# Kernel tuning notes

Measured on AMD Instinct MI355X. Metric: run time of the kernel, lower is better.

Reference implementation:

```python
import jax, jax.numpy as jnp
import numpy as np

# Scalar-only irreps: 8x0e nodes in, 4x0e edge in, 8x0e edge out, 16x0e node out.
N = 50000          # nodes
E = 800000         # edges
MUL_NODE_IN = 8
MUL_EDGE_IN = 4
MUL_Z = 2 * MUL_NODE_IN          # cat([x[i], x[j]]) -> 16
MUL_EDGE_OUT = 8
MUL_NODE_OUT = 16
W_NUMEL = MUL_EDGE_IN * MUL_Z * MUL_EDGE_OUT  # 512 = edge_tp.weight_numel
RAD_IN, RAD_HID = 16, 64         # radial_neurons=[16, 64]


def setup_inputs() -> dict:
    key = jax.random.key(0)
    ks = jax.random.split(key, 7)
    x = jax.random.normal(ks[0], (N, MUL_NODE_IN), dtype=jnp.float32)
    edge_index = jax.random.randint(ks[1], (2, E), 0, N)
    edge_attr = jax.random.normal(ks[2], (E, MUL_EDGE_IN), dtype=jnp.float32)
    edge_len_emb = jax.random.normal(ks[3], (E, RAD_IN), dtype=jnp.float32)
    # radial MLP (e3nn FullyConnectedNet: normalized linear layers, silu)
    w1 = jax.random.normal(ks[4], (RAD_IN, RAD_HID), dtype=jnp.float32)
    w2 = jax.random.normal(ks[5], (RAD_HID, W_NUMEL), dtype=jnp.float32)
    # node_tp internal shared weights: [mul_node_in, mul_edge_out, mul_node_out]
    w_node = jax.random.normal(ks[6], (MUL_NODE_IN, MUL_EDGE_OUT, MUL_NODE_OUT), dtype=jnp.float32)
    return {"x": x, "edge_index": edge_index, "edge_attr": edge_attr,
            "edge_len_emb": edge_len_emb, "w1": w1, "w2": w2, "w_node": w_node}


def reference(x, edge_index, edge_attr, edge_len_emb, w1, w2, w_node):
    i, j = edge_index[0], edge_index[1]
    # radial MLP -> per-edge TP weights (e3nn normalized linears, silu)
    h = jax.nn.silu(edge_len_emb @ w1 / jnp.sqrt(jnp.float32(RAD_IN)))
    w_edge = (h @ w2 / jnp.sqrt(jnp.float32(RAD_HID)))
    w_edge = w_edge.reshape(E, MUL_EDGE_IN, MUL_Z, MUL_EDGE_OUT)
    # gather + concat: z = cat([x[i], x[j]])  [E, 16]
    z = jnp.concatenate([x[i], x[j]], axis=-1)
    # edge_tp: fully-connected scalar TP with path norm 1/sqrt(mul1*mul2)
    edge_out = jnp.einsum('ea,eb,eabk->ek', edge_attr, z, w_edge)
    edge_out = edge_out / jnp.sqrt(jnp.float32(MUL_EDGE_IN * MUL_Z))
    # scatter-sum to destination nodes j
    e_sum = jax.ops.segment_sum(edge_out, j, num_segments=x.shape[0])
    # node_tp: shared internal weights, path norm 1/sqrt(mul1*mul2)
    x_out = jnp.einsum('na,nb,abk->nk', x, e_sum, w_node)
    x_out = x_out / jnp.sqrt(jnp.float32(MUL_NODE_IN * MUL_EDGE_OUT))
    return (x_out, edge_out)
```

## Files before the change

kernel.cpp:

```cpp
#include <hip/hip_runtime.h>


typedef __attribute__((ext_vector_type(8))) short short8;
typedef __attribute__((ext_vector_type(4))) float floatx4;

__device__ inline unsigned short f2bf(float f) {
    union { float f; unsigned u; } v; v.f = f;
    unsigned r = v.u + 0x7FFFu + ((v.u >> 16) & 1u);
    return (unsigned short)(r >> 16);
}

__device__ inline unsigned cvt_pk_bf16(float lo, float hi) {
    unsigned r;
    asm("v_cvt_pk_bf16_f32 %0, %1, %2" : "=v"(r) : "v"(lo), "v"(hi));
    return r;
}

constexpr int TB   = 512;
constexpr int NBLK = 256;

constexpr int W2_LD  = 72;
constexpr int HS_LD  = 72;
constexpr int ZT_LDF = 48;
constexpr int AT_LDF = 32;

__global__ __launch_bounds__(TB, 2) void edge_kernel(
    const float* __restrict__ x,
    const int*   __restrict__ ei,
    const float* __restrict__ attr,
    const float* __restrict__ emb,
    const float* __restrict__ w1,
    const float* __restrict__ w2,
    float* __restrict__ edge_out,
    float* __restrict__ e_sum,
    int E)
{
    __shared__ __align__(16) unsigned short s_w2t[512 * W2_LD];
    __shared__ __align__(16) unsigned short s_hsA[8 * 32 * HS_LD];
    __shared__ __align__(16) float          s_ztA[8 * 16 * ZT_LDF];
    __shared__ __align__(16) float          s_atA[8 * 4 * AT_LDF];
    __shared__ int                          s_vjA[8 * 32];

    const int tid  = threadIdx.x;
    const int wave = tid >> 6;
    const int lane = tid & 63;
    const int m16  = lane & 15;
    const int quad = lane >> 4;
    const int par  = m16 >> 3;

    for (int idx = tid; idx < 512 * 64; idx += TB) {
        const int n = idx & 511, k = idx >> 9;
        s_w2t[n * W2_LD + k] = f2bf(w2[k * 512 + n]);
    }
    __syncthreads();

    short8 w1f[4];
    #pragma unroll
    for (int ct = 0; ct < 4; ++ct) {
        short8 f;
        if (quad < 2) {
            #pragma unroll
            for (int j = 0; j < 8; ++j)
                f[j] = (short)f2bf(w1[(quad * 8 + j) * 64 + ct * 16 + m16]);
        } else {
            #pragma unroll
            for (int j = 0; j < 8; ++j) f[j] = 0;
        }
        w1f[ct] = f;
    }

    unsigned short* hsw = s_hsA + wave * 32 * HS_LD;
    float*          ztw = s_ztA + wave * 16 * ZT_LDF;
    float*          atw = s_atA + wave * 4 * AT_LDF;
    int*            vjw = s_vjA + wave * 32;

    const int  wid = blockIdx.x * 8 + wave;
    const int  nw  = NBLK * 8;
    const int  ntiles = E >> 5;
    const bool stg = (quad < 2);
    const int  mst = quad * 16 + m16;

    float4 xi0, xi1, xj0, xj1, a4;
    float4 em0a, em0b, em1a, em1b;
    int viN = 0, vjN = 0, vjC = 0;

    if (wid < ntiles && stg) {
        const int e0 = (wid << 5) + mst;
        const int vi = ei[e0];
        vjC = ei[E + e0];
        xi0 = *(const float4*)(x + (size_t)vi * 8);
        xi1 = *(const float4*)(x + (size_t)vi * 8 + 4);
        xj0 = *(const float4*)(x + (size_t)vjC * 8);
        xj1 = *(const float4*)(x + (size_t)vjC * 8 + 4);
        a4  = *(const float4*)(attr + (size_t)e0 * 4);
        const float* ep0 = emb + (size_t)((wid << 5) + m16) * 16 + quad * 8;
        em0a = *(const float4*)ep0;
        em0b = *(const float4*)(ep0 + 4);
        const float* ep1 = emb + (size_t)((wid << 5) + 16 + m16) * 16 + quad * 8;
        em1a = *(const float4*)ep1;
        em1b = *(const float4*)(ep1 + 4);
        const int t1 = (wid + nw < ntiles) ? (wid + nw) : wid;
        const int e1 = (t1 << 5) + mst;
        viN = ei[e1];
        vjN = ei[E + e1];
    }

    for (int tile = wid; tile < ntiles; tile += nw) {
        const int base = tile << 5;

        if (stg) {
            ztw[ 0*ZT_LDF+mst]=xi0.x; ztw[ 1*ZT_LDF+mst]=xi0.y;
            ztw[ 2*ZT_LDF+mst]=xi0.z; ztw[ 3*ZT_LDF+mst]=xi0.w;
            ztw[ 4*ZT_LDF+mst]=xi1.x; ztw[ 5*ZT_LDF+mst]=xi1.y;
            ztw[ 6*ZT_LDF+mst]=xi1.z; ztw[ 7*ZT_LDF+mst]=xi1.w;
            ztw[ 8*ZT_LDF+mst]=xj0.x; ztw[ 9*ZT_LDF+mst]=xj0.y;
            ztw[10*ZT_LDF+mst]=xj0.z; ztw[11*ZT_LDF+mst]=xj0.w;
            ztw[12*ZT_LDF+mst]=xj1.x; ztw[13*ZT_LDF+mst]=xj1.y;
            ztw[14*ZT_LDF+mst]=xj1.z; ztw[15*ZT_LDF+mst]=xj1.w;
            atw[0*AT_LDF+mst]=a4.x;   atw[1*AT_LDF+mst]=a4.y;
            atw[2*AT_LDF+mst]=a4.z;   atw[3*AT_LDF+mst]=a4.w;
            vjw[mst] = vjC;
        }

        short8 a1[2];
        {
            union { short8 s8; unsigned u[4]; } uu;
            if (stg) {
                uu.u[0] = cvt_pk_bf16(em0a.x, em0a.y);
                uu.u[1] = cvt_pk_bf16(em0a.z, em0a.w);
                uu.u[2] = cvt_pk_bf16(em0b.x, em0b.y);
                uu.u[3] = cvt_pk_bf16(em0b.z, em0b.w);
            } else {
                uu.u[0]=0u; uu.u[1]=0u; uu.u[2]=0u; uu.u[3]=0u;
            }
            a1[0] = uu.s8;
            if (stg) {
                uu.u[0] = cvt_pk_bf16(em1a.x, em1a.y);
                uu.u[1] = cvt_pk_bf16(em1a.z, em1a.w);
                uu.u[2] = cvt_pk_bf16(em1b.x, em1b.y);
                uu.u[3] = cvt_pk_bf16(em1b.z, em1b.w);
            } else {
                uu.u[0]=0u; uu.u[1]=0u; uu.u[2]=0u; uu.u[3]=0u;
            }
            a1[1] = uu.s8;
        }

        {
            const int tn     = tile + nw;
            const int tn_cl  = (tn  < ntiles) ? tn  : tile;
            const int tnn    = tn + nw;
            const int tnn_cl = (tnn < ntiles) ? tnn : tn_cl;
            if (stg) {
                const int en = (tn_cl << 5) + mst;
                vjC = vjN;
                xi0 = *(const float4*)(x + (size_t)viN * 8);
                xi1 = *(const float4*)(x + (size_t)viN * 8 + 4);
                xj0 = *(const float4*)(x + (size_t)vjN * 8);
                xj1 = *(const float4*)(x + (size_t)vjN * 8 + 4);
                a4  = *(const float4*)(attr + (size_t)en * 4);
                const float* ep0 = emb + (size_t)((tn_cl << 5) + m16) * 16 + quad * 8;
                em0a = *(const float4*)ep0;
                em0b = *(const float4*)(ep0 + 4);
                const float* ep1 = emb + (size_t)((tn_cl << 5) + 16 + m16) * 16 + quad * 8;
                em1a = *(const float4*)ep1;
                em1b = *(const float4*)(ep1 + 4);
                const int enn = (tnn_cl << 5) + mst;
                viN = ei[enn];
                vjN = ei[E + enn];
            }
        }

        #pragma unroll
        for (int s = 0; s < 2; ++s) {
            #pragma unroll
            for (int ct = 0; ct < 4; ++ct) {
                floatx4 c = {0.f, 0.f, 0.f, 0.f};
                c = __builtin_amdgcn_mfma_f32_16x16x32_bf16(a1[s], w1f[ct], c, 0, 0, 0);
                float sv[4];
                #pragma unroll
                for (int r = 0; r < 4; ++r) {
                    const float u   = c[r] * 0.25f;
                    const float den = 1.f + __expf(-u);
                    sv[r] = u * __builtin_amdgcn_rcpf(den) * 0.015625f;
                }
                const unsigned p01 = cvt_pk_bf16(sv[0], sv[1]);
                const unsigned p23 = cvt_pk_bf16(sv[2], sv[3]);
                const int col  = ct * 16 + m16;
                const int row0 = s * 16 + quad * 4;
                hsw[(row0 + 0) * HS_LD + col] = (unsigned short)p01;
                hsw[(row0 + 1) * HS_LD + col] = (unsigned short)(p01 >> 16);
                hsw[(row0 + 2) * HS_LD + col] = (unsigned short)p23;
                hsw[(row0 + 3) * HS_LD + col] = (unsigned short)(p23 >> 16);
            }
        }

        short8 a2[2][2];
        #pragma unroll
        for (int s = 0; s < 2; ++s)
            #pragma unroll
            for (int q = 0; q < 2; ++q)
                a2[s][q] = *(const short8*)(hsw + (s * 16 + m16) * HS_LD + q * 32 + quad * 8);

        float eacc[2][4];
        #pragma unroll
        for (int s = 0; s < 2; ++s)
            #pragma unroll
            for (int r = 0; r < 4; ++r) eacc[s][r] = 0.f;

        __builtin_amdgcn_s_setprio(1);
        #pragma unroll 1
        for (int g = 0; g < 4; ++g) {
            float av[2][4];
            #pragma unroll
            for (int s = 0; s < 2; ++s) {
                const float4 a4v = *(const float4*)(atw + g * AT_LDF + s * 16 + quad * 4);
                av[s][0] = a4v.x; av[s][1] = a4v.y;
                av[s][2] = a4v.z; av[s][3] = a4v.w;
            }
            float tacc[2][4];
            #pragma unroll
            for (int s = 0; s < 2; ++s)
                #pragma unroll
                for (int r = 0; r < 4; ++r) tacc[s][r] = 0.f;

            #pragma unroll
            for (int tt = 0; tt < 8; ++tt) {
                const int t = g * 8 + tt;
                short8 b2[2];
                b2[0] = *(const short8*)(s_w2t + (16 * t + m16) * W2_LD + quad * 8);
                b2[1] = *(const short8*)(s_w2t + (16 * t + m16) * W2_LD + 32 + quad * 8);
                const int b_idx = (2 * tt + par) & 15;
                #pragma unroll
                for (int s = 0; s < 2; ++s) {
                    floatx4 c = {0.f, 0.f, 0.f, 0.f};
                    c = __builtin_amdgcn_mfma_f32_16x16x32_bf16(a2[s][0], b2[0], c, 0, 0, 0);
                    c = __builtin_amdgcn_mfma_f32_16x16x32_bf16(a2[s][1], b2[1], c, 0, 0, 0);
                    const float4 zv = *(const float4*)(ztw + b_idx * ZT_LDF + s * 16 + quad * 4);
                    tacc[s][0] = fmaf(c[0], zv.x, tacc[s][0]);
                    tacc[s][1] = fmaf(c[1], zv.y, tacc[s][1]);
                    tacc[s][2] = fmaf(c[2], zv.z, tacc[s][2]);
                    tacc[s][3] = fmaf(c[3], zv.w, tacc[s][3]);
                }
            }
            #pragma unroll
            for (int s = 0; s < 2; ++s)
                #pragma unroll
                for (int r = 0; r < 4; ++r)
                    eacc[s][r] = fmaf(av[s][r], tacc[s][r], eacc[s][r]);
        }
        __builtin_amdgcn_s_setprio(0);

        #pragma unroll
        for (int s = 0; s < 2; ++s)
            #pragma unroll
            for (int r = 0; r < 4; ++r)
                eacc[s][r] += __shfl_xor(eacc[s][r], 8, 64);

        if (m16 < 8) {
            #pragma unroll
            for (int s = 0; s < 2; ++s) {
                const int4 vjq = *(const int4*)(vjw + s * 16 + quad * 4);
                const int vjr[4] = {vjq.x, vjq.y, vjq.z, vjq.w};
                #pragma unroll
                for (int r = 0; r < 4; ++r) {
                    const int e = base + s * 16 + quad * 4 + r;
                    edge_out[(size_t)e * 8 + m16] = eacc[s][r];
                    atomicAdd(e_sum + (size_t)vjr[r] * 8 + m16, eacc[s][r]);
                }
            }
        }
    }
}

__global__ __launch_bounds__(256) void node_kernel(
    const float* __restrict__ x,
    const float* __restrict__ e_sum,
    const float* __restrict__ w_node,
    float* __restrict__ x_out,
    int N)
{
    __shared__ float s_w[8 * 8 * 16];
    for (int idx = threadIdx.x; idx < 1024; idx += 256) s_w[idx] = w_node[idx];
    __syncthreads();

    const int n = blockIdx.x * 256 + threadIdx.x;
    if (n >= N) return;

    float xa[8], eb[8];
    #pragma unroll
    for (int a = 0; a < 8; ++a) xa[a] = x[(size_t)n * 8 + a];
    #pragma unroll
    for (int b = 0; b < 8; ++b) eb[b] = e_sum[(size_t)n * 8 + b];

    float out[16];
    #pragma unroll
    for (int k = 0; k < 16; ++k) out[k] = 0.f;

    const float4* wv = (const float4*)s_w;
    #pragma unroll
    for (int a = 0; a < 8; ++a) {
        #pragma unroll
        for (int b = 0; b < 8; ++b) {
            const float t = xa[a] * eb[b] * 0.125f;
            #pragma unroll
            for (int k4 = 0; k4 < 4; ++k4) {
                const float4 w = wv[(a * 8 + b) * 4 + k4];
                out[k4 * 4 + 0] = fmaf(t, w.x, out[k4 * 4 + 0]);
                out[k4 * 4 + 1] = fmaf(t, w.y, out[k4 * 4 + 1]);
                out[k4 * 4 + 2] = fmaf(t, w.z, out[k4 * 4 + 2]);
                out[k4 * 4 + 3] = fmaf(t, w.w, out[k4 * 4 + 3]);
            }
        }
    }

    float4* xo = (float4*)(x_out + (size_t)n * 16);
    #pragma unroll
    for (int k4 = 0; k4 < 4; ++k4)
        xo[k4] = make_float4(out[k4 * 4 + 0], out[k4 * 4 + 1],
                             out[k4 * 4 + 2], out[k4 * 4 + 3]);
}

extern "C" void kernel_launch(void* const* d_in, const int* in_sizes, int n_in,
                              void* d_out, int out_size, void* d_ws, size_t ws_size,
                              hipStream_t stream) {
    const float* x      = (const float*)d_in[0];
    const int*   ei     = (const int*)d_in[1];
    const float* attr   = (const float*)d_in[2];
    const float* emb    = (const float*)d_in[3];
    const float* w1     = (const float*)d_in[4];
    const float* w2     = (const float*)d_in[5];
    const float* w_node = (const float*)d_in[6];

    const int N = in_sizes[0] / 8;
    const int E = in_sizes[2] / 4;

    float* x_out    = (float*)d_out;
    float* edge_out = (float*)d_out + (size_t)N * 16;
    float* e_sum    = (float*)d_ws;

    hipMemsetAsync(e_sum, 0, (size_t)N * 8 * sizeof(float), stream);

    edge_kernel<<<NBLK, TB, 0, stream>>>(x, ei, attr, emb, w1, w2,
                                         edge_out, e_sum, E);

    node_kernel<<<(N + 255) / 256, 256, 0, stream>>>(x, e_sum, w_node, x_out, N);
}
```

Before: 190.8 us.

## Cut edge kernel LDS via swizzled w2 layout and register shuffles; raise occupancy

```diff
diff --git a/kernel.cpp b/kernel.cpp
--- a/kernel.cpp
+++ b/kernel.cpp
@@ -17,14 +17,9 @@
 }
 
 constexpr int TB   = 512;
-constexpr int NBLK = 256;
-
-constexpr int W2_LD  = 72;
-constexpr int HS_LD  = 72;
-constexpr int ZT_LDF = 48;
-constexpr int AT_LDF = 32;
-
-__global__ __launch_bounds__(TB, 2) void edge_kernel(
+constexpr int NBLK = 512;
+
+__global__ __launch_bounds__(TB, 4) void edge_kernel(
     const float* __restrict__ x,
     const int*   __restrict__ ei,
     const float* __restrict__ attr,
@@ -35,11 +30,8 @@
     float* __restrict__ e_sum,
     int E)
 {
-    __shared__ __align__(16) unsigned short s_w2t[512 * W2_LD];
-    __shared__ __align__(16) unsigned short s_hsA[8 * 32 * HS_LD];
-    __shared__ __align__(16) float          s_ztA[8 * 16 * ZT_LDF];
-    __shared__ __align__(16) float          s_atA[8 * 4 * AT_LDF];
-    __shared__ int                          s_vjA[8 * 32];
+    __shared__ __align__(16) unsigned short s_w2t[512 * 64];
+    __shared__ __align__(16) float          s_ztA[8 * 16 * 32];
 
     const int tid  = threadIdx.x;
     const int wave = tid >> 6;
@@ -50,35 +42,39 @@
 
     for (int idx = tid; idx < 512 * 64; idx += TB) {
         const int n = idx & 511, k = idx >> 9;
-        s_w2t[n * W2_LD + k] = f2bf(w2[k * 512 + n]);
+        s_w2t[n * 64 + (k ^ ((n & 7) << 3))] = f2bf(w2[k * 512 + n]);
     }
     __syncthreads();
 
     short8 w1f[4];
     #pragma unroll
-    for (int ct = 0; ct < 4; ++ct) {
+    for (int mt = 0; mt < 4; ++mt) {
         short8 f;
         if (quad < 2) {
             #pragma unroll
             for (int j = 0; j < 8; ++j)
-                f[j] = (short)f2bf(w1[(quad * 8 + j) * 64 + ct * 16 + m16]);
+                f[j] = (short)f2bf(w1[(quad * 8 + j) * 64 + mt * 16 + m16]);
         } else {
             #pragma unroll
             for (int j = 0; j < 8; ++j) f[j] = 0;
         }
-        w1f[ct] = f;
-    }
-
-    unsigned short* hsw = s_hsA + wave * 32 * HS_LD;
-    float*          ztw = s_ztA + wave * 16 * ZT_LDF;
-    float*          atw = s_atA + wave * 4 * AT_LDF;
-    int*            vjw = s_vjA + wave * 32;
+        w1f[mt] = f;
+    }
+
+    float* ztw = s_ztA + wave * 16 * 32;
 
     const int  wid = blockIdx.x * 8 + wave;
     const int  nw  = NBLK * 8;
     const int  ntiles = E >> 5;
     const bool stg = (quad < 2);
     const int  mst = quad * 16 + m16;
+
+    const int srcA = m16 + 16 * ((2 * quad) & 3);
+    const int srcB = m16 + 16 * ((2 * quad + 1) & 3);
+
+    const int swz = (m16 & 7) << 3;
+    const int o0  = (quad * 8) ^ swz;
+    const int o1  = o0 ^ 32;
 
     float4 xi0, xi1, xj0, xj1, a4;
     float4 em0a, em0b, em1a, em1b;
@@ -109,18 +105,17 @@
         const int base = tile << 5;
 
         if (stg) {
-            ztw[ 0*ZT_LDF+mst]=xi0.x; ztw[ 1*ZT_LDF+mst]=xi0.y;
-            ztw[ 2*ZT_LDF+mst]=xi0.z; ztw[ 3*ZT_LDF+mst]=xi0.w;
-            ztw[ 4*ZT_LDF+mst]=xi1.x; ztw[ 5*ZT_LDF+mst]=xi1.y;
-            ztw[ 6*ZT_LDF+mst]=xi1.z; ztw[ 7*ZT_LDF+mst]=xi1.w;
-            ztw[ 8*ZT_LDF+mst]=xj0.x; ztw[ 9*ZT_LDF+mst]=xj0.y;
-            ztw[10*ZT_LDF+mst]=xj0.z; ztw[11*ZT_LDF+mst]=xj0.w;
-            ztw[12*ZT_LDF+mst]=xj1.x; ztw[13*ZT_LDF+mst]=xj1.y;
-            ztw[14*ZT_LDF+mst]=xj1.z; ztw[15*ZT_LDF+mst]=xj1.w;
-            atw[0*AT_LDF+mst]=a4.x;   atw[1*AT_LDF+mst]=a4.y;
-            atw[2*AT_LDF+mst]=a4.z;   atw[3*AT_LDF+mst]=a4.w;
-            vjw[mst] = vjC;
-        }
+            ztw[ 0*32+mst]=xi0.x; ztw[ 1*32+mst]=xi0.y;
+            ztw[ 2*32+mst]=xi0.z; ztw[ 3*32+mst]=xi0.w;
+            ztw[ 4*32+mst]=xi1.x; ztw[ 5*32+mst]=xi1.y;
+            ztw[ 6*32+mst]=xi1.z; ztw[ 7*32+mst]=xi1.w;
+            ztw[ 8*32+mst]=xj0.x; ztw[ 9*32+mst]=xj0.y;
+            ztw[10*32+mst]=xj0.z; ztw[11*32+mst]=xj0.w;
+            ztw[12*32+mst]=xj1.x; ztw[13*32+mst]=xj1.y;
+            ztw[14*32+mst]=xj1.z; ztw[15*32+mst]=xj1.w;
+        }
+        const float4 a4cur = a4;
+        const int    vjE   = vjC;
 
         short8 a1[2];
         {
@@ -170,36 +165,41 @@
             }
         }
 
+        short8 a2[2][2];
         #pragma unroll
         for (int s = 0; s < 2; ++s) {
-            #pragma unroll
-            for (int ct = 0; ct < 4; ++ct) {
-                floatx4 c = {0.f, 0.f, 0.f, 0.f};
-                c = __builtin_amdgcn_mfma_f32_16x16x32_bf16(a1[s], w1f[ct], c, 0, 0, 0);
+            floatx4 c[4];
+            #pragma unroll
+            for (int mt = 0; mt < 4; ++mt) {
+                floatx4 z4 = {0.f, 0.f, 0.f, 0.f};
+                c[mt] = __builtin_amdgcn_mfma_f32_16x16x32_bf16(w1f[mt], a1[s], z4, 0, 0, 0);
+            }
+            unsigned p[4][2];
+            #pragma unroll
+            for (int mt = 0; mt < 4; ++mt) {
                 float sv[4];
                 #pragma unroll
                 for (int r = 0; r < 4; ++r) {
-                    const float u   = c[r] * 0.25f;
+                    const float u   = c[mt][r] * 0.25f;
                     const float den = 1.f + __expf(-u);
                     sv[r] = u * __builtin_amdgcn_rcpf(den) * 0.015625f;
                 }
-                const unsigned p01 = cvt_pk_bf16(sv[0], sv[1]);
-                const unsigned p23 = cvt_pk_bf16(sv[2], sv[3]);
-                const int col  = ct * 16 + m16;
-                const int row0 = s * 16 + quad * 4;
-                hsw[(row0 + 0) * HS_LD + col] = (unsigned short)p01;
-                hsw[(row0 + 1) * HS_LD + col] = (unsigned short)(p01 >> 16);
-                hsw[(row0 + 2) * HS_LD + col] = (unsigned short)p23;
-                hsw[(row0 + 3) * HS_LD + col] = (unsigned short)(p23 >> 16);
-            }
-        }
-
-        short8 a2[2][2];
-        #pragma unroll
-        for (int s = 0; s < 2; ++s)
-            #pragma unroll
-            for (int q = 0; q < 2; ++q)
-                a2[s][q] = *(const short8*)(hsw + (s * 16 + m16) * HS_LD + q * 32 + quad * 8);
+                p[mt][0] = cvt_pk_bf16(sv[0], sv[1]);
+                p[mt][1] = cvt_pk_bf16(sv[2], sv[3]);
+            }
+            #pragma unroll
+            for (int qq = 0; qq < 2; ++qq) {
+                union { short8 s8; unsigned u[4]; } uu;
+                #pragma unroll
+                for (int w = 0; w < 4; ++w) {
+                    const int srcLane = (w < 2) ? srcA : srcB;
+                    const unsigned vA = (unsigned)__shfl((int)p[2*qq    ][w & 1], srcLane, 64);
+                    const unsigned vB = (unsigned)__shfl((int)p[2*qq + 1][w & 1], srcLane, 64);
+                    uu.u[w] = (quad & 2) ? vB : vA;
+                }
+                a2[s][qq] = uu.s8;
+            }
+        }
 
         float eacc[2][4];
         #pragma unroll
@@ -210,13 +210,15 @@
         __builtin_amdgcn_s_setprio(1);
         #pragma unroll 1
         for (int g = 0; g < 4; ++g) {
+            const float ag = (g == 0) ? a4cur.x : (g == 1) ? a4cur.y
+                           : (g == 2) ? a4cur.z : a4cur.w;
             float av[2][4];
             #pragma unroll
-            for (int s = 0; s < 2; ++s) {
-                const float4 a4v = *(const float4*)(atw + g * AT_LDF + s * 16 + quad * 4);
-                av[s][0] = a4v.x; av[s][1] = a4v.y;
-                av[s][2] = a4v.z; av[s][3] = a4v.w;
-            }
+            for (int s = 0; s < 2; ++s)
+                #pragma unroll
+                for (int r = 0; r < 4; ++r)
+                    av[s][r] = __shfl(ag, s * 16 + quad * 4 + r, 64);
+
             float tacc[2][4];
             #pragma unroll
             for (int s = 0; s < 2; ++s)
@@ -226,16 +228,17 @@
             #pragma unroll
             for (int tt = 0; tt < 8; ++tt) {
                 const int t = g * 8 + tt;
+                const unsigned short* wrow = s_w2t + (16 * t + m16) * 64;
                 short8 b2[2];
-                b2[0] = *(const short8*)(s_w2t + (16 * t + m16) * W2_LD + quad * 8);
-                b2[1] = *(const short8*)(s_w2t + (16 * t + m16) * W2_LD + 32 + quad * 8);
+                b2[0] = *(const short8*)(wrow + o0);
+                b2[1] = *(const short8*)(wrow + o1);
                 const int b_idx = (2 * tt + par) & 15;
                 #pragma unroll
                 for (int s = 0; s < 2; ++s) {
                     floatx4 c = {0.f, 0.f, 0.f, 0.f};
                     c = __builtin_amdgcn_mfma_f32_16x16x32_bf16(a2[s][0], b2[0], c, 0, 0, 0);
                     c = __builtin_amdgcn_mfma_f32_16x16x32_bf16(a2[s][1], b2[1], c, 0, 0, 0);
-                    const float4 zv = *(const float4*)(ztw + b_idx * ZT_LDF + s * 16 + quad * 4);
+                    const float4 zv = *(const float4*)(ztw + b_idx * 32 + s * 16 + quad * 4);
                     tacc[s][0] = fmaf(c[0], zv.x, tacc[s][0]);
                     tacc[s][1] = fmaf(c[1], zv.y, tacc[s][1]);
                     tacc[s][2] = fmaf(c[2], zv.z, tacc[s][2]);
@@ -256,16 +259,21 @@
             for (int r = 0; r < 4; ++r)
                 eacc[s][r] += __shfl_xor(eacc[s][r], 8, 64);
 
+        int vjr[2][4];
+        #pragma unroll
+        for (int s = 0; s < 2; ++s)
+            #pragma unroll
+            for (int r = 0; r < 4; ++r)
+                vjr[s][r] = __shfl(vjE, s * 16 + quad * 4 + r, 64);
+
         if (m16 < 8) {
             #pragma unroll
             for (int s = 0; s < 2; ++s) {
-                const int4 vjq = *(const int4*)(vjw + s * 16 + quad * 4);
-                const int vjr[4] = {vjq.x, vjq.y, vjq.z, vjq.w};
                 #pragma unroll
                 for (int r = 0; r < 4; ++r) {
                     const int e = base + s * 16 + quad * 4 + r;
                     edge_out[(size_t)e * 8 + m16] = eacc[s][r];
-                    atomicAdd(e_sum + (size_t)vjr[r] * 8 + m16, eacc[s][r]);
+                    atomicAdd(e_sum + (size_t)vjr[s][r] * 8 + m16, eacc[s][r]);
                 }
             }
         }
```

Measured after the change: 439.1 us. 130% more time.
